# Optimization experiments

Hardware: AMD Instinct MI355X
Metric: run time of the kernel (lower is better)

Reference implementation:

```python
import jax, jax.numpy as jnp
import numpy as np

ALPHA = 0.2   # LeakyReLU slope
V = 7         # graph nodes (hard-coded 7x7 adjacency in source)
BN_EPS = 1e-5


def _leaky(x):
    return jnp.where(x >= 0, x, ALPHA * x)


def _norm_adj(B):
    # adj = min-max normalized (B + I), then D^{-1/2} adj D^{-1/2}
    adj = B + jnp.eye(V, dtype=B.dtype)
    adj = (adj - adj.min()) / (adj.max() - adj.min())
    inv = 1.0 / jnp.sqrt(jnp.sum(adj, axis=1))
    return adj * inv[:, None] * inv[None, :]


def _gat1_head(h_flat, W, a, B):
    # h_flat: (N, V, C*T)=  (N,7,180); W: (180,9); a: (18,1); B: (7,7)
    Wh = h_flat @ W                       # (N, V, E)
    E = W.shape[1]
    s_i = Wh @ a[:E, 0]                   # (N, V)  == [Wh_i ; .] part of concat score
    s_j = Wh @ a[E:, 0]                   # (N, V)  == [. ; Wh_j] part
    e = _leaky(s_i[:, :, None] + s_j[:, None, :])   # (N, V, V)
    att = jax.nn.softmax(e, axis=-1)
    adjn = _norm_adj(B)
    att = jnp.einsum('ik,nkj->nij', adjn, att)      # adj_norm @ attention
    return jax.nn.elu(att @ Wh)           # (N, V, E)


def _gat2_head(h, W, a, B):
    # h: (N, V, C, 30); W: (30,10); a: (20,1); B: (7,7)
    Wh = h @ W                            # (N, V, C, F)
    F = W.shape[1]
    s_i = jnp.einsum('nvcf,f->nvc', Wh, a[:F, 0])
    s_j = jnp.einsum('nvcf,f->nvc', Wh, a[F:, 0])
    e = _leaky(s_i[:, :, None, :] + s_j[:, None, :, :])   # (N, V, V, C)
    att = jax.nn.softmax(e, axis=-1)      # softmax over channel dim (as in source)
    # nested V-loop with diag_embed == weighted sum over j, per-channel scaling
    h2 = jnp.einsum('njcf,nijc->ncfi', Wh, att)           # (N, C, F, V)
    adjn = _norm_adj(B)
    out = jnp.einsum('ncfu,uv->ncfv', h2, adjn)
    return jax.nn.elu(out)                # (N, C, F, V)


def setup_inputs() -> dict:
    key = jax.random.key(0)
    ks = jax.random.split(key, 16)
    N, C, T = 32768, 6, 30
    f32 = jnp.float32
    inp = {
        'x': jax.random.normal(ks[0], (N, C, T, V), f32),
        'bn_gamma': jax.random.uniform(ks[1], (42,), f32, 0.5, 1.5),
        'bn_beta': 0.1 * jax.random.normal(ks[2], (42,), f32),
        'W1': 0.1 * jax.random.normal(ks[3], (20, 180, 9), f32),
        'a1': 0.1 * jax.random.normal(ks[4], (20, 18, 1), f32),
        'B1': 0.01 * jax.random.uniform(ks[5], (20, V, V), f32) + 1e-6,
        'W2': 0.1 * jax.random.normal(ks[6], (3, 30, 10), f32),
        'a2': 0.1 * jax.random.normal(ks[7], (3, 20, 1), f32),
        'B2': 0.01 * jax.random.uniform(ks[8], (3, V, V), f32) + 1e-6,
        'W_ih': 0.1 * jax.random.normal(ks[9], (84, 84), f32),
        'W_hh': 0.1 * jax.random.normal(ks[10], (84, 21), f32),
        'b_ih': 0.1 * jax.random.normal(ks[11], (84,), f32),
        'b_hh': 0.1 * jax.random.normal(ks[12], (84,), f32),
        'W_out': 0.1 * jax.random.normal(ks[13], (7, 21), f32),
        'b_out': 0.1 * jax.random.normal(ks[14], (7,), f32),
    }
    return inp


def reference(x, bn_gamma, bn_beta, W1, a1, B1, W2, a2, B2,
              W_ih, W_hh, b_ih, b_hh, W_out, b_out):
    N, C, T, _ = x.shape                  # (N, 6, 30, 7)
    # data_bn: BatchNorm1d(42) in train mode (batch stats over N and T)
    xb = jnp.transpose(x, (0, 3, 1, 2)).reshape(N, V * C, T)
    mean = jnp.mean(xb, axis=(0, 2), keepdims=True)
    var = jnp.var(xb, axis=(0, 2), keepdims=True)
    xb = (xb - mean) / jnp.sqrt(var + BN_EPS)
    xb = xb * bn_gamma[None, :, None] + bn_beta[None, :, None]
    x0 = jnp.transpose(xb.reshape(N, V, C, T), (0, 2, 3, 1))   # (N, C, T, V)

    # l1: 20-head GAT on flattened (C*T) node features
    h_flat = jnp.transpose(x0, (0, 3, 1, 2)).reshape(N, V, C * T)
    heads1 = jax.vmap(_gat1_head, in_axes=(None, 0, 0, 0))(h_flat, W1, a1, B1)  # (20,N,V,9)
    x1 = jnp.moveaxis(heads1, 0, 2).reshape(N, V, C * T)       # cat over heads, last dim
    x1 = jnp.transpose(x1.reshape(N, V, C, T), (0, 2, 3, 1))   # (N, C, T, V)

    # l2: 3-head 2D GAT over the T axis
    h2in = jnp.transpose(x0, (0, 3, 1, 2))                      # (N, V, C, T)
    heads2 = jax.vmap(_gat2_head, in_axes=(None, 0, 0, 0))(h2in, W2, a2, B2)  # (3,N,C,10,V)
    x2 = jnp.moveaxis(heads2, 0, 2).reshape(N, C, 30, V)        # cat over heads on dim=2

    xcat = jnp.concatenate([x1, x2], axis=1)                    # (N, 12, 30, 7)

    # RNN head: source takes r_out[:, 0, :], so only LSTM step 0 (h0=c0=0) matters
    xs = jnp.transpose(xcat, (0, 2, 1, 3)).reshape(N, T, 84)
    gates = xs[:, 0, :] @ W_ih.T + b_ih + b_hh                  # h0=0 => W_hh term vanishes
    i_g, f_g, g_g, o_g = jnp.split(gates, 4, axis=-1)           # torch gate order i,f,g,o
    c1 = jax.nn.sigmoid(i_g) * jnp.tanh(g_g)
    h1 = jax.nn.sigmoid(o_g) * jnp.tanh(c1)
    return h1 @ W_out.T + b_out                                 # (N, 7)
```

## Files before the change

### kernel.cpp

```cpp
#include <hip/hip_runtime.h>

#define F1260 1260
#define NPART 512
#define PB_OFF (NPART * 84)

__device__ __forceinline__ float leakyf(float x) { return x >= 0.f ? x : 0.2f * x; }
__device__ __forceinline__ float eluf(float x) { return x > 0.f ? x : expm1f(x); }
__device__ __forceinline__ float sigmoidf(float x) { return 1.f / (1.f + __expf(-x)); }
__device__ __forceinline__ float tanh_fast(float x) { return 1.f - 2.f / (__expf(2.f * x) + 1.f); }


__global__ __launch_bounds__(320) void kA_stats(const float* __restrict__ x,
                                                float* __restrict__ ws, int rows) {
    __shared__ float fs[1260], fq[1260];
    const int t = threadIdx.x;
    const int n0 = blockIdx.x * rows;
    if (t < 315) {
        const int f0 = t * 4;
        float s0 = 0.f, s1 = 0.f, s2 = 0.f, s3 = 0.f;
        float q0 = 0.f, q1 = 0.f, q2 = 0.f, q3 = 0.f;
#pragma unroll 16
        for (int i = 0; i < rows; ++i) {
            const float4 a = *(const float4*)(x + (size_t)(n0 + i) * F1260 + f0);
            s0 += a.x; q0 += a.x * a.x;
            s1 += a.y; q1 += a.y * a.y;
            s2 += a.z; q2 += a.z * a.z;
            s3 += a.w; q3 += a.w * a.w;
        }
        fs[f0 + 0] = s0; fq[f0 + 0] = q0;
        fs[f0 + 1] = s1; fq[f0 + 1] = q1;
        fs[f0 + 2] = s2; fq[f0 + 2] = q2;
        fs[f0 + 3] = s3; fq[f0 + 3] = q3;
    }
    __syncthreads();
    if (t < 42) {
        const int v = t / 6, c = t % 6;
        float s = 0.f, q = 0.f;
#pragma unroll
        for (int tt = 0; tt < 30; ++tt) {
            const int f = c * 210 + tt * 7 + v;
            s += fs[f];
            q += fq[f];
        }
        ws[blockIdx.x * 84 + t] = s;
        ws[blockIdx.x * 84 + 42 + t] = q;
    }
}

__global__ __launch_bounds__(384) void kB_setup(
        const float* __restrict__ bn_gamma, const float* __restrict__ bn_beta,
        const float* __restrict__ W1, const float* __restrict__ a1, const float* __restrict__ B1,
        const float* __restrict__ W2, const float* __restrict__ a2, const float* __restrict__ B2,
        const float* __restrict__ b_ih, const float* __restrict__ b_hh,
        const float* __restrict__ W_out, const float* __restrict__ b_out,
        float* __restrict__ ws, int N) {
    __shared__ float red[336];
    const int t = threadIdx.x;
    float* pb = ws + PB_OFF;
    const int HH[6] = {0, 3, 6, 10, 13, 16};
    const int EH[6] = {0, 3, 6, 0, 3, 6};

    if (t < 336) {
        const int part = t / 84, slot = t - part * 84;
        const int b0 = part * (NPART / 4);
        float s = 0.f;
#pragma unroll 8
        for (int b = 0; b < NPART / 4; ++b) s += ws[(size_t)(b0 + b) * 84 + slot];
        red[t] = s;
    }
    __syncthreads();
    if (t < 42) {
        const float s = red[t] + red[84 + t] + red[168 + t] + red[252 + t];
        const float q = red[42 + t] + red[126 + t] + red[210 + t] + red[294 + t];
        const float cnt = 30.f * (float)N;
        const float mean = s / cnt;
        const float var = q / cnt - mean * mean;
        const float sc = bn_gamma[t] * rsqrtf(var + 1e-5f);
        pb[t] = sc;
        pb[64 + t] = bn_beta[t] - mean * sc;
    }
    if (t >= 64 && t < 71) {
        const int idx = t - 64;
        const float* Bp = (idx < 6) ? (B1 + HH[idx] * 49) : B2;
        float* op = pb + 128 + idx * 49;
        float adj[49];
        for (int i = 0; i < 49; ++i) adj[i] = Bp[i];
        for (int i = 0; i < 7; ++i) adj[i * 8] += 1.f;
        float mn = adj[0], mx = adj[0];
        for (int i = 1; i < 49; ++i) { mn = fminf(mn, adj[i]); mx = fmaxf(mx, adj[i]); }
        const float inv = 1.f / (mx - mn);
        float rinv[7];
        for (int i = 0; i < 7; ++i) {
            float rs = 0.f;
            for (int j = 0; j < 7; ++j) { adj[i * 7 + j] = (adj[i * 7 + j] - mn) * inv; rs += adj[i * 7 + j]; }
            rinv[i] = rsqrtf(rs);
        }
        for (int i = 0; i < 7; ++i)
            for (int j = 0; j < 7; ++j)
                op[i * 7 + j] = adj[i * 7 + j] * rinv[i] * rinv[j];
    }
    for (int task = t; task < 6 * 180; task += 384) {
        const int hh = task / 180, k = task % 180;
        const int h = HH[hh];
        const float* Wp = W1 + ((size_t)h * 180 + k) * 9;
        float si = 0.f, sj = 0.f;
        for (int e = 0; e < 9; ++e) {
            const float w = Wp[e];
            si += w * a1[h * 18 + e];
            sj += w * a1[h * 18 + 9 + e];
        }
        pb[512 + k * 21 + hh * 3 + 0] = si;
        pb[512 + k * 21 + hh * 3 + 1] = sj;
        pb[512 + k * 21 + hh * 3 + 2] = Wp[EH[hh]];
    }
    if (t < 30) {
        const float* Wp = W2 + t * 10;
        float si = 0.f, sj = 0.f;
        for (int f = 0; f < 10; ++f) {
            const float w = Wp[f];
            si += w * a2[f];
            sj += w * a2[10 + f];
        }
        for (int c = 0; c < 6; ++c) {
            const int k = c * 30 + t;
            pb[512 + k * 21 + 18] = si;
            pb[512 + k * 21 + 19] = sj;
            pb[512 + k * 21 + 20] = Wp[0];
        }
    }
    if (t < 84) pb[4832 + t] = b_ih[t] + b_hh[t];
    if (t < 147) pb[4928 + t] = W_out[t];
    if (t < 7) pb[5078 + t] = b_out[t];
}

#define RS 252
__global__ __launch_bounds__(128) void kC_main(const float* __restrict__ x,
        const float* __restrict__ pb, const float* __restrict__ Wih,
        float* __restrict__ outp, int N) {
    __shared__ __align__(16) float sm[4459];
    float* res  = sm;
    float* scsh = sm + 4032;
    float* adjL = sm + 4116;

    const int t = threadIdx.x;
    const int n0 = blockIdx.x * 16;
    const int v = (t >> 3) & 7;
    const int nl = ((t >> 6) << 3) + (t & 7);

    for (int i = t; i < 84; i += 128) scsh[i] = pb[i < 42 ? i : 22 + i];
    for (int i = t; i < 343; i += 128) adjL[i] = pb[128 + i];
    __syncthreads();

    if (v < 7) {
        float s1[18];
#pragma unroll
        for (int i = 0; i < 18; ++i) s1[i] = 0.f;
        const float* xb = x + (size_t)(n0 + nl) * F1260 + v;
        const float* WB = pb + 512;
        for (int c = 0; c < 6; ++c) {
            const float sc = scsh[v * 6 + c];
            const float sh = scsh[42 + v * 6 + c];
            const float* xr = xb + c * 210;
            const float* wb = WB + (c * 30) * 21;
            float xv[30];
#pragma unroll
            for (int tt = 0; tt < 30; ++tt) xv[tt] = xr[tt * 7];
            float g0 = 0.f, g1 = 0.f, g2 = 0.f;
#pragma unroll
            for (int tt = 0; tt < 30; ++tt) {
                const float a = xv[tt] * sc + sh;
                const float* w = wb + tt * 21;
#pragma unroll
                for (int q = 0; q < 18; ++q) s1[q] += a * w[q];
                g0 += a * w[18];
                g1 += a * w[19];
                g2 += a * w[20];
            }
            float* rp = res + nl * RS + 126 + (v * 6 + c) * 3;
            rp[0] = g0; rp[1] = g1; rp[2] = g2;
        }
#pragma unroll
        for (int q = 0; q < 18; ++q)
            res[nl * RS + v * 18 + q] = s1[q];
    }
    __syncthreads();

    const int hh = v;
    float si[7], sj[7], we[7];
#pragma unroll
    for (int vv = 0; vv < 7; ++vv) {
        const float* rp = res + nl * RS + vv * 18 + hh * 3;
        si[vv] = rp[0]; sj[vv] = rp[1]; we[vv] = rp[2];
    }
    __syncthreads();
    if (hh < 6) {
        float mxsj = sj[0];
#pragma unroll
        for (int j = 1; j < 7; ++j) mxsj = fmaxf(mxsj, sj[j]);
        float p[7];
#pragma unroll
        for (int i = 0; i < 7; ++i) {
            const float m = leakyf(si[i] + mxsj);
            float den = 0.f, num = 0.f;
#pragma unroll
            for (int j = 0; j < 7; ++j) {
                const float w = __expf(leakyf(si[i] + sj[j]) - m);
                den += w;
                num += w * we[j];
            }
            p[i] = num / den;
        }
        const float* An = adjL + hh * 49;
#pragma unroll
        for (int i = 0; i < 7; ++i) {
            float r = 0.f;
#pragma unroll
            for (int k = 0; k < 7; ++k) r += An[i * 7 + k] * p[k];
            res[nl * RS + hh * 7 + i] = eluf(r);
        }
    }
    if (v < 7) {
        const int i = v;
        float si2[6];
#pragma unroll
        for (int c = 0; c < 6; ++c)
            si2[c] = res[nl * RS + 126 + (i * 6 + c) * 3];
        float hc[6];
#pragma unroll
        for (int c = 0; c < 6; ++c) hc[c] = 0.f;
#pragma unroll
        for (int j = 0; j < 7; ++j) {
            float s[6];
            float m = -1e30f;
#pragma unroll
            for (int c = 0; c < 6; ++c) {
                const float* rp = res + nl * RS + 126 + (j * 6 + c) * 3;
                s[c] = leakyf(si2[c] + rp[1]);
                m = fmaxf(m, s[c]);
            }
            float den = 0.f;
#pragma unroll
            for (int c = 0; c < 6; ++c) { s[c] = __expf(s[c] - m); den += s[c]; }
            const float rd = 1.f / den;
#pragma unroll
            for (int c = 0; c < 6; ++c) {
                const float wh0 = res[nl * RS + 126 + (j * 6 + c) * 3 + 2];
                hc[c] += wh0 * s[c] * rd;
            }
        }
#pragma unroll
        for (int c = 0; c < 6; ++c)
            res[nl * RS + 84 + i * 6 + c] = hc[c];
    }
    __syncthreads();

    if (v < 6) {
        const int c = v;
        const float* An2 = adjL + 6 * 49;
        float h[7];
#pragma unroll
        for (int u = 0; u < 7; ++u) h[u] = res[nl * RS + 84 + u * 6 + c];
#pragma unroll
        for (int vv = 0; vv < 7; ++vv) {
            float r = 0.f;
#pragma unroll
            for (int u = 0; u < 7; ++u) r += h[u] * An2[u * 7 + vv];
            res[nl * RS + 42 + c * 7 + vv] = eluf(r);
        }
    }
    __syncthreads();

    {
        const int g8 = v;
        const float* bias = pb + 4832;
        const float4* xs4 = (const float4*)(res + nl * RS);
        for (int gi = g8; gi < 21; gi += 8) {
            float ga = bias[gi], gg = bias[42 + gi], go = bias[63 + gi];
            const float4* wa = (const float4*)(Wih + gi * 84);
            const float4* wg = (const float4*)(Wih + (42 + gi) * 84);
            const float4* wo = (const float4*)(Wih + (63 + gi) * 84);
#pragma unroll
            for (int k = 0; k < 21; ++k) {
                const float4 xv = xs4[k];
                const float4 a4 = wa[k];
                const float4 g4 = wg[k];
                const float4 o4 = wo[k];
                ga += xv.x * a4.x + xv.y * a4.y + xv.z * a4.z + xv.w * a4.w;
                gg += xv.x * g4.x + xv.y * g4.y + xv.z * g4.z + xv.w * g4.w;
                go += xv.x * o4.x + xv.y * o4.y + xv.z * o4.z + xv.w * o4.w;
            }
            const float c1 = sigmoidf(ga) * tanh_fast(gg);
            res[nl * RS + 126 + gi] = sigmoidf(go) * tanh_fast(c1);
        }
    }
    __syncthreads();

    if (t < 112) {
        const int n5 = t / 7, j = t - n5 * 7;
        const float* Wout = pb + 4928;
        float r = pb[5078 + j];
#pragma unroll
        for (int m = 0; m < 21; ++m) r += res[n5 * RS + 126 + m] * Wout[j * 21 + m];
        outp[(size_t)n0 * 7 + t] = r;
    }
}

extern "C" void kernel_launch(void* const* d_in, const int* in_sizes, int n_in,
                              void* d_out, int out_size, void* d_ws, size_t ws_size,
                              hipStream_t stream) {
    const int N = in_sizes[0] / F1260;

    const float* x        = (const float*)d_in[0];
    const float* bn_gamma = (const float*)d_in[1];
    const float* bn_beta  = (const float*)d_in[2];
    const float* W1       = (const float*)d_in[3];
    const float* a1       = (const float*)d_in[4];
    const float* B1       = (const float*)d_in[5];
    const float* W2       = (const float*)d_in[6];
    const float* a2       = (const float*)d_in[7];
    const float* B2       = (const float*)d_in[8];
    const float* W_ih     = (const float*)d_in[9];
    const float* b_ih     = (const float*)d_in[11];
    const float* b_hh     = (const float*)d_in[12];
    const float* W_out    = (const float*)d_in[13];
    const float* b_out    = (const float*)d_in[14];

    float* wsf = (float*)d_ws;


    kA_stats<<<dim3(NPART), dim3(320), 0, stream>>>(x, wsf, N / NPART);
    kB_setup<<<dim3(1), dim3(384), 0, stream>>>(bn_gamma, bn_beta, W1, a1, B1,
                                                W2, a2, B2, b_ih, b_hh,
                                                W_out, b_out, wsf, N);
    kC_main<<<dim3(N / 16), dim3(128), 0, stream>>>(x, wsf + PB_OFF, W_ih,
                                                    (float*)d_out, N);
}
```

Before: 341.0 us.

## Fuse stats, setup and main passes into one cooperative persistent kernel

Replaces the three-kernel sequence (BN statistics, parameter setup, main GAT/LSTM pass) with a single cooperative kernel of 1024 blocks that uses grid-wide syncs between phases and then loops persistently over the 16-sample groups. The goal is to remove kernel launch gaps and the single-block setup kernel's serialization, and to get some L2 reuse of x between the stats pass and the main pass. The cost is three grid.sync barriers, fewer resident blocks (1024 x 128 threads) for the main compute, and a weaker stats reduction with less parallelism per block. If the cooperative launch fails, the code falls back to the old three-kernel path.

```diff
diff --git a/kernel.cpp b/kernel.cpp
--- a/kernel.cpp
+++ b/kernel.cpp
@@ -1,14 +1,323 @@
 #include <hip/hip_runtime.h>
+#include <hip/hip_cooperative_groups.h>
+
+namespace cg = cooperative_groups;
 
 #define F1260 1260
-#define NPART 512
-#define PB_OFF (NPART * 84)
 
 __device__ __forceinline__ float leakyf(float x) { return x >= 0.f ? x : 0.2f * x; }
 __device__ __forceinline__ float eluf(float x) { return x > 0.f ? x : expm1f(x); }
 __device__ __forceinline__ float sigmoidf(float x) { return 1.f / (1.f + __expf(-x)); }
 __device__ __forceinline__ float tanh_fast(float x) { return 1.f - 2.f / (__expf(2.f * x) + 1.f); }
 
+#define FG 1024
+#define TOT_OFF 86016
+#define FPB_OFF 86272
+#define RS 252
+
+struct KP {
+    const float *x, *bn_gamma, *bn_beta, *W1, *a1, *B1, *W2, *a2, *B2;
+    const float *Wih, *b_ih, *b_hh, *W_out, *b_out;
+    float *ws, *out;
+    int N;
+};
+
+__global__ __launch_bounds__(128) void kFused(KP p) {
+    __shared__ __align__(16) float sm[4459];
+    float* res  = sm;
+    float* scsh = sm + 4032;
+    float* adjL = sm + 4116;
+
+    const int t = threadIdx.x;
+    const int b = blockIdx.x;
+    cg::grid_group grid = cg::this_grid();
+    float* ws = p.ws;
+    float* pb = ws + FPB_OFF;
+    const int rowsS = p.N / FG;
+
+    {
+        float* fs = sm;
+        float* fq = sm + 1260;
+        const int n0 = b * rowsS;
+        for (int q = t; q < 315; q += 128) {
+            float s0 = 0.f, s1 = 0.f, s2 = 0.f, s3 = 0.f;
+            float q0 = 0.f, q1 = 0.f, q2 = 0.f, q3 = 0.f;
+#pragma unroll 8
+            for (int i = 0; i < rowsS; ++i) {
+                const float4 a = *(const float4*)(p.x + (size_t)(n0 + i) * F1260 + q * 4);
+                s0 += a.x; q0 += a.x * a.x;
+                s1 += a.y; q1 += a.y * a.y;
+                s2 += a.z; q2 += a.z * a.z;
+                s3 += a.w; q3 += a.w * a.w;
+            }
+            fs[q * 4 + 0] = s0; fq[q * 4 + 0] = q0;
+            fs[q * 4 + 1] = s1; fq[q * 4 + 1] = q1;
+            fs[q * 4 + 2] = s2; fq[q * 4 + 2] = q2;
+            fs[q * 4 + 3] = s3; fq[q * 4 + 3] = q3;
+        }
+        __syncthreads();
+        if (t < 42) {
+            const int v = t / 6, c = t % 6;
+            float s = 0.f, q = 0.f;
+#pragma unroll
+            for (int tt = 0; tt < 30; ++tt) {
+                const int f = c * 210 + tt * 7 + v;
+                s += fs[f];
+                q += fq[f];
+            }
+            ws[(size_t)t * FG + b] = s;
+            ws[(size_t)(42 + t) * FG + b] = q;
+        }
+    }
+    grid.sync();
+
+    if (b < 84) {
+        const float* src = ws + (size_t)b * FG;
+        float s = 0.f;
+        for (int i = t; i < FG; i += 128) s += src[i];
+        sm[t] = s;
+        __syncthreads();
+        for (int off = 64; off >= 1; off >>= 1) {
+            if (t < off) sm[t] += sm[t + off];
+            __syncthreads();
+        }
+        if (t == 0) ws[TOT_OFF + b] = sm[0];
+    }
+    grid.sync();
+
+    if (b == 0) {
+        const int HH[6] = {0, 3, 6, 10, 13, 16};
+        const int EH[6] = {0, 3, 6, 0, 3, 6};
+        if (t < 42) {
+            const float cnt = 30.f * (float)p.N;
+            const float mean = ws[TOT_OFF + t] / cnt;
+            const float var = ws[TOT_OFF + 42 + t] / cnt - mean * mean;
+            const float sc = p.bn_gamma[t] * rsqrtf(var + 1e-5f);
+            pb[t] = sc;
+            pb[64 + t] = p.bn_beta[t] - mean * sc;
+        }
+        if (t >= 64 && t < 71) {
+            const int idx = t - 64;
+            const float* Bp = (idx < 6) ? (p.B1 + HH[idx] * 49) : p.B2;
+            float* op = pb + 128 + idx * 49;
+            float adj[49];
+            for (int i = 0; i < 49; ++i) adj[i] = Bp[i];
+            for (int i = 0; i < 7; ++i) adj[i * 8] += 1.f;
+            float mn = adj[0], mx = adj[0];
+            for (int i = 1; i < 49; ++i) { mn = fminf(mn, adj[i]); mx = fmaxf(mx, adj[i]); }
+            const float inv = 1.f / (mx - mn);
+            float rinv[7];
+            for (int i = 0; i < 7; ++i) {
+                float rs = 0.f;
+                for (int j = 0; j < 7; ++j) { adj[i * 7 + j] = (adj[i * 7 + j] - mn) * inv; rs += adj[i * 7 + j]; }
+                rinv[i] = rsqrtf(rs);
+            }
+            for (int i = 0; i < 7; ++i)
+                for (int j = 0; j < 7; ++j)
+                    op[i * 7 + j] = adj[i * 7 + j] * rinv[i] * rinv[j];
+        }
+        for (int task = t; task < 6 * 180; task += 128) {
+            const int hh = task / 180, k = task % 180;
+            const int h = HH[hh];
+            const float* Wp = p.W1 + ((size_t)h * 180 + k) * 9;
+            float si = 0.f, sj = 0.f;
+            for (int e = 0; e < 9; ++e) {
+                const float w = Wp[e];
+                si += w * p.a1[h * 18 + e];
+                sj += w * p.a1[h * 18 + 9 + e];
+            }
+            pb[512 + k * 21 + hh * 3 + 0] = si;
+            pb[512 + k * 21 + hh * 3 + 1] = sj;
+            pb[512 + k * 21 + hh * 3 + 2] = Wp[EH[hh]];
+        }
+        if (t < 30) {
+            const float* Wp = p.W2 + t * 10;
+            float si = 0.f, sj = 0.f;
+            for (int f = 0; f < 10; ++f) {
+                const float w = Wp[f];
+                si += w * p.a2[f];
+                sj += w * p.a2[10 + f];
+            }
+            for (int c = 0; c < 6; ++c) {
+                const int k = c * 30 + t;
+                pb[512 + k * 21 + 18] = si;
+                pb[512 + k * 21 + 19] = sj;
+                pb[512 + k * 21 + 20] = Wp[0];
+            }
+        }
+        if (t < 84) pb[4832 + t] = p.b_ih[t] + p.b_hh[t];
+        for (int i = t; i < 147; i += 128) pb[4928 + i] = p.W_out[i];
+        if (t < 7) pb[5078 + t] = p.b_out[t];
+    }
+    grid.sync();
+
+    const int v = (t >> 3) & 7;
+    const int nl = ((t >> 6) << 3) + (t & 7);
+    for (int i = t; i < 84; i += 128) scsh[i] = pb[i < 42 ? i : 22 + i];
+    for (int i = t; i < 343; i += 128) adjL[i] = pb[128 + i];
+
+    const int ngroups = p.N / 16;
+    for (int g = b; g < ngroups; g += FG) {
+        __syncthreads();
+        const int n0 = g * 16;
+
+        if (v < 7) {
+            float s1[18];
+#pragma unroll
+            for (int i = 0; i < 18; ++i) s1[i] = 0.f;
+            const float* xb = p.x + (size_t)(n0 + nl) * F1260 + v;
+            const float* WB = pb + 512;
+            for (int c = 0; c < 6; ++c) {
+                const float sc = scsh[v * 6 + c];
+                const float sh = scsh[42 + v * 6 + c];
+                const float* xr = xb + c * 210;
+                const float* wb = WB + (c * 30) * 21;
+                float xv[30];
+#pragma unroll
+                for (int tt = 0; tt < 30; ++tt) xv[tt] = xr[tt * 7];
+                float g0 = 0.f, g1 = 0.f, g2 = 0.f;
+#pragma unroll
+                for (int tt = 0; tt < 30; ++tt) {
+                    const float a = xv[tt] * sc + sh;
+                    const float* w = wb + tt * 21;
+#pragma unroll
+                    for (int q = 0; q < 18; ++q) s1[q] += a * w[q];
+                    g0 += a * w[18];
+                    g1 += a * w[19];
+                    g2 += a * w[20];
+                }
+                float* rp = res + nl * RS + 126 + (v * 6 + c) * 3;
+                rp[0] = g0; rp[1] = g1; rp[2] = g2;
+            }
+#pragma unroll
+            for (int q = 0; q < 18; ++q)
+                res[nl * RS + v * 18 + q] = s1[q];
+        }
+        __syncthreads();
+
+        const int hh = v;
+        float si[7], sj[7], we[7];
+#pragma unroll
+        for (int vv = 0; vv < 7; ++vv) {
+            const float* rp = res + nl * RS + vv * 18 + hh * 3;
+            si[vv] = rp[0]; sj[vv] = rp[1]; we[vv] = rp[2];
+        }
+        __syncthreads();
+        if (hh < 6) {
+            float mxsj = sj[0];
+#pragma unroll
+            for (int j = 1; j < 7; ++j) mxsj = fmaxf(mxsj, sj[j]);
+            float pr[7];
+#pragma unroll
+            for (int i = 0; i < 7; ++i) {
+                const float m = leakyf(si[i] + mxsj);
+                float den = 0.f, num = 0.f;
+#pragma unroll
+                for (int j = 0; j < 7; ++j) {
+                    const float w = __expf(leakyf(si[i] + sj[j]) - m);
+                    den += w;
+                    num += w * we[j];
+                }
+                pr[i] = num / den;
+            }
+            const float* An = adjL + hh * 49;
+#pragma unroll
+            for (int i = 0; i < 7; ++i) {
+                float r = 0.f;
+#pragma unroll
+                for (int k = 0; k < 7; ++k) r += An[i * 7 + k] * pr[k];
+                res[nl * RS + hh * 7 + i] = eluf(r);
+            }
+        }
+        if (v < 7) {
+            const int i = v;
+            float si2[6];
+#pragma unroll
+            for (int c = 0; c < 6; ++c)
+                si2[c] = res[nl * RS + 126 + (i * 6 + c) * 3];
+            float hc[6];
+#pragma unroll
+            for (int c = 0; c < 6; ++c) hc[c] = 0.f;
+#pragma unroll
+            for (int j = 0; j < 7; ++j) {
+                float s[6];
+                float m = -1e30f;
+#pragma unroll
+                for (int c = 0; c < 6; ++c) {
+                    const float* rp = res + nl * RS + 126 + (j * 6 + c) * 3;
+                    s[c] = leakyf(si2[c] + rp[1]);
+                    m = fmaxf(m, s[c]);
+                }
+                float den = 0.f;
+#pragma unroll
+                for (int c = 0; c < 6; ++c) { s[c] = __expf(s[c] - m); den += s[c]; }
+                const float rd = 1.f / den;
+#pragma unroll
+                for (int c = 0; c < 6; ++c) {
+                    const float wh0 = res[nl * RS + 126 + (j * 6 + c) * 3 + 2];
+                    hc[c] += wh0 * s[c] * rd;
+                }
+            }
+#pragma unroll
+            for (int c = 0; c < 6; ++c)
+                res[nl * RS + 84 + i * 6 + c] = hc[c];
+        }
+        __syncthreads();
+
+        if (v < 6) {
+            const int c = v;
+            const float* An2 = adjL + 6 * 49;
+            float h[7];
+#pragma unroll
+            for (int u = 0; u < 7; ++u) h[u] = res[nl * RS + 84 + u * 6 + c];
+#pragma unroll
+            for (int vv = 0; vv < 7; ++vv) {
+                float r = 0.f;
+#pragma unroll
+                for (int u = 0; u < 7; ++u) r += h[u] * An2[u * 7 + vv];
+                res[nl * RS + 42 + c * 7 + vv] = eluf(r);
+            }
+        }
+        __syncthreads();
+
+        {
+            const int g8 = v;
+            const float* bias = pb + 4832;
+            const float4* xs4 = (const float4*)(res + nl * RS);
+            for (int gi = g8; gi < 21; gi += 8) {
+                float ga = bias[gi], gg = bias[42 + gi], go = bias[63 + gi];
+                const float4* wa = (const float4*)(p.Wih + gi * 84);
+                const float4* wg = (const float4*)(p.Wih + (42 + gi) * 84);
+                const float4* wo = (const float4*)(p.Wih + (63 + gi) * 84);
+#pragma unroll
+                for (int k = 0; k < 21; ++k) {
+                    const float4 xv = xs4[k];
+                    const float4 a4 = wa[k];
+                    const float4 g4 = wg[k];
+                    const float4 o4 = wo[k];
+                    ga += xv.x * a4.x + xv.y * a4.y + xv.z * a4.z + xv.w * a4.w;
+                    gg += xv.x * g4.x + xv.y * g4.y + xv.z * g4.z + xv.w * g4.w;
+                    go += xv.x * o4.x + xv.y * o4.y + xv.z * o4.z + xv.w * o4.w;
+                }
+                const float c1 = sigmoidf(ga) * tanh_fast(gg);
+                res[nl * RS + 126 + gi] = sigmoidf(go) * tanh_fast(c1);
+            }
+        }
+        __syncthreads();
+
+        if (t < 112) {
+            const int n5 = t / 7, j = t - n5 * 7;
+            const float* Wout = pb + 4928;
+            float r = pb[5078 + j];
+#pragma unroll
+            for (int m = 0; m < 21; ++m) r += res[n5 * RS + 126 + m] * Wout[j * 21 + m];
+            p.out[(size_t)n0 * 7 + t] = r;
+        }
+    }
+}
+
+#define NPART 512
+#define PB_OFF (NPART * 84)
 
 __global__ __launch_bounds__(320) void kA_stats(const float* __restrict__ x,
                                                 float* __restrict__ ws, int rows) {
@@ -133,7 +442,6 @@
     if (t < 7) pb[5078 + t] = b_out[t];
 }
 
-#define RS 252
 __global__ __launch_bounds__(128) void kC_main(const float* __restrict__ x,
         const float* __restrict__ pb, const float* __restrict__ Wih,
         float* __restrict__ outp, int N) {
@@ -197,7 +505,7 @@
         float mxsj = sj[0];
 #pragma unroll
         for (int j = 1; j < 7; ++j) mxsj = fmaxf(mxsj, sj[j]);
-        float p[7];
+        float pr[7];
 #pragma unroll
         for (int i = 0; i < 7; ++i) {
             const float m = leakyf(si[i] + mxsj);
@@ -208,14 +516,14 @@
                 den += w;
                 num += w * we[j];
             }
-            p[i] = num / den;
+            pr[i] = num / den;
         }
         const float* An = adjL + hh * 49;
 #pragma unroll
         for (int i = 0; i < 7; ++i) {
             float r = 0.f;
 #pragma unroll
-            for (int k = 0; k < 7; ++k) r += An[i * 7 + k] * p[k];
+            for (int k = 0; k < 7; ++k) r += An[i * 7 + k] * pr[k];
             res[nl * RS + hh * 7 + i] = eluf(r);
         }
     }
@@ -327,11 +635,23 @@
 
     float* wsf = (float*)d_ws;
 
-
-    kA_stats<<<dim3(NPART), dim3(320), 0, stream>>>(x, wsf, N / NPART);
-    kB_setup<<<dim3(1), dim3(384), 0, stream>>>(bn_gamma, bn_beta, W1, a1, B1,
-                                                W2, a2, B2, b_ih, b_hh,
-                                                W_out, b_out, wsf, N);
-    kC_main<<<dim3(N / 16), dim3(128), 0, stream>>>(x, wsf + PB_OFF, W_ih,
-                                                    (float*)d_out, N);
+    hipError_t e = hipErrorUnknown;
+    const bool okFused = (N % FG == 0) && (N % 16 == 0) &&
+                         (ws_size >= (size_t)(FPB_OFF + 5085 + 64) * sizeof(float));
+    if (okFused) {
+        KP p = { x, bn_gamma, bn_beta, W1, a1, B1, W2, a2, B2,
+                 W_ih, b_ih, b_hh, W_out, b_out, wsf, (float*)d_out, N };
+        void* args[] = { &p };
+        e = hipLaunchCooperativeKernel((void*)kFused, dim3(FG), dim3(128),
+                                       args, 0, stream);
+    }
+    if (e != hipSuccess) {
+        (void)hipGetLastError();
+        kA_stats<<<dim3(NPART), dim3(320), 0, stream>>>(x, wsf, N / NPART);
+        kB_setup<<<dim3(1), dim3(384), 0, stream>>>(bn_gamma, bn_beta, W1, a1, B1,
+                                                    W2, a2, B2, b_ih, b_hh,
+                                                    W_out, b_out, wsf, N);
+        kC_main<<<dim3(N / 16), dim3(128), 0, stream>>>(x, wsf + PB_OFF, W_ih,
+                                                        (float*)d_out, N);
+    }
 }
```

Measured after the change: 810.8 us. +137.8%, slower.
